# Optimization experiments

Measured on AMD Instinct MI355X. Metric: run time of the kernel, lower is better.

## Reference

```python
import jax, jax.numpy as jnp
import numpy as np

B, DM, E, P, K = 8192, 512, 4, 1024, 2
F = DM * E  # fused_input_dim = 2048


def setup_inputs() -> dict:
    key = jax.random.key(0)
    ks = jax.random.split(key, 8)
    return {
        "x_mod0": jax.random.normal(ks[0], (B, DM), jnp.float32),
        "x_mod1": jax.random.normal(ks[1], (B, DM), jnp.float32),
        "x_mod2": jax.random.normal(ks[2], (B, DM), jnp.float32),
        "x_mod3": jax.random.normal(ks[3], (B, DM), jnp.float32),
        "label": jax.random.normal(ks[4], (B, P), jnp.float32),
        "Wg": jax.random.normal(ks[5], (E, F), jnp.float32) * (1.0 / np.sqrt(F)),
        "We": jax.random.normal(ks[6], (E, F, P), jnp.float32) * (1.0 / np.sqrt(F)),
        "be": jax.random.normal(ks[7], (E, P), jnp.float32) * 0.01,
        "topk": K,
    }


def reference(x_mod0, x_mod1, x_mod2, x_mod3, label, Wg, We, be, topk):
    # fused = cat(modalities, dim=1)  -> [B, F]
    fused = jnp.concatenate([x_mod0, x_mod1, x_mod2, x_mod3], axis=1)
    # gate_scores = softmax(Linear(fused))  (Linear weight is [out,in], no bias)
    gate_scores = jax.nn.softmax(fused @ Wg.T, axis=-1)  # [B, E]
    top_k_values, top_k_indices = jax.lax.top_k(gate_scores, topk)  # [B, K]
    # Dense equivalent of per-sample expert dispatch: run every expert,
    # then gather the top-k expert outputs per token and weighted-sum them.
    all_out = jnp.einsum("bf,efp->bep", fused, We) + be  # [B, E, P]
    gathered = jnp.take_along_axis(all_out, top_k_indices[:, :, None], axis=1)  # [B, K, P]
    preds = jnp.sum(gathered * top_k_values[:, :, None], axis=1)  # [B, P]
    # loss_fn = MSE against x['label']
    loss = jnp.mean((preds - label) ** 2)
    return (loss, preds)
```

## Files before the change

kernel.cpp:

```cpp
#include <hip/hip_runtime.h>
#include <stdint.h>

#define Bsz  8192
#define DMOD 512
#define NE   4
#define NP   1024
#define NF   2048
#define BM   160
#define MAXTILES 57

typedef float  f32x4  __attribute__((ext_vector_type(4)));
typedef __bf16 bf16x8 __attribute__((ext_vector_type(8)));
typedef unsigned short u16x8 __attribute__((ext_vector_type(8)));

typedef __attribute__((address_space(3))) void       lds_void;
typedef const __attribute__((address_space(1))) void glb_void;
#define GLOAD16(gp, lp) \
  __builtin_amdgcn_global_load_lds((glb_void*)(gp), (lds_void*)(lp), 16, 0, 0)

__device__ __forceinline__ unsigned short f32_bf16(float f) {
  unsigned int u = __float_as_uint(f);
  u += 0x7FFFu + ((u >> 16) & 1u);
  return (unsigned short)(u >> 16);
}

__global__ __launch_bounds__(256) void gate_fuse(
    const float* __restrict__ x0, const float* __restrict__ x1,
    const float* __restrict__ x2, const float* __restrict__ x3,
    const float* __restrict__ Wg, const float* __restrict__ We,
    float* __restrict__ gw, int* __restrict__ pair,
    unsigned short* __restrict__ fusedB, unsigned short* __restrict__ WeT)
{
  __shared__ float sred[4][4];
  __shared__ float tsh[64][65];
  const int tid = threadIdx.x;

  if ((int)blockIdx.x < Bsz) {
    const int b = blockIdx.x;
    const int f = tid * 8;
    const float* xm  = (f < 1024) ? (f < 512 ? x0 : x1) : (f < 1536 ? x2 : x3);
    const float* src = xm + (size_t)b * DMOD + (f & 511);
    float4 v0 = *(const float4*)src;
    float4 v1 = *(const float4*)(src + 4);
    u16x8 o;
    o[0] = f32_bf16(v0.x); o[1] = f32_bf16(v0.y); o[2] = f32_bf16(v0.z); o[3] = f32_bf16(v0.w);
    o[4] = f32_bf16(v1.x); o[5] = f32_bf16(v1.y); o[6] = f32_bf16(v1.z); o[7] = f32_bf16(v1.w);
    *(u16x8*)(fusedB + (size_t)b * NF + f) = o;

    float d[4];
    #pragma unroll
    for (int e = 0; e < 4; ++e) {
      const float* w = Wg + e * NF + f;
      d[e] = v0.x * w[0] + v0.y * w[1] + v0.z * w[2] + v0.w * w[3]
           + v1.x * w[4] + v1.y * w[5] + v1.z * w[6] + v1.w * w[7];
    }
    #pragma unroll
    for (int off = 32; off; off >>= 1) {
      #pragma unroll
      for (int e = 0; e < 4; ++e) d[e] += __shfl_xor(d[e], off);
    }
    if ((tid & 63) == 0) {
      #pragma unroll
      for (int e = 0; e < 4; ++e) sred[tid >> 6][e] = d[e];
    }
    __syncthreads();
    if (tid == 0) {
      float a0 = sred[0][0] + sred[1][0] + sred[2][0] + sred[3][0];
      float a1 = sred[0][1] + sred[1][1] + sred[2][1] + sred[3][1];
      float a2 = sred[0][2] + sred[1][2] + sred[2][2] + sred[3][2];
      float a3 = sred[0][3] + sred[1][3] + sred[2][3] + sred[3][3];
      float m  = fmaxf(fmaxf(a0, a1), fmaxf(a2, a3));
      float e0 = expf(a0 - m), e1 = expf(a1 - m), e2 = expf(a2 - m), e3 = expf(a3 - m);
      float inv = 1.f / (e0 + e1 + e2 + e3);
      float p0 = e0 * inv, p1 = e1 * inv, p2 = e2 * inv, p3 = e3 * inv;
      int i1 = 0; float b1 = a0;
      if (a1 > b1) { b1 = a1; i1 = 1; }
      if (a2 > b1) { b1 = a2; i1 = 2; }
      if (a3 > b1) { b1 = a3; i1 = 3; }
      int i2 = -1; float b2 = -3.4e38f;
      if (i1 != 0 && a0 > b2) { b2 = a0; i2 = 0; }
      if (i1 != 1 && a1 > b2) { b2 = a1; i2 = 1; }
      if (i1 != 2 && a2 > b2) { b2 = a2; i2 = 2; }
      if (i1 != 3 && a3 > b2) { b2 = a3; i2 = 3; }
      gw[(size_t)b * 4 + 0] = (i1 == 0 || i2 == 0) ? p0 : 0.f;
      gw[(size_t)b * 4 + 1] = (i1 == 1 || i2 == 1) ? p1 : 0.f;
      gw[(size_t)b * 4 + 2] = (i1 == 2 || i2 == 2) ? p2 : 0.f;
      gw[(size_t)b * 4 + 3] = (i1 == 3 || i2 == 3) ? p3 : 0.f;
      int lo = min(i1, i2), hi = max(i1, i2);
      pair[b] = (lo == 0) ? (hi - 1) : (lo == 1) ? (hi + 1) : 5;
    }
  } else {
    const int tb = (int)blockIdx.x - Bsz;
    const int e  = tb >> 9;
    const int rem = tb & 511;
    const int tf = (rem & 31) * 64;
    const int tp = (rem >> 5) * 64;
    const int t4 = tid * 4;
    const float* src = We + ((size_t)e * NF + tf) * NP + tp;
    #pragma unroll
    for (int i = 0; i < 4; ++i) {
      int li = i * 1024 + t4;
      int r = li >> 6, c = li & 63;
      float4 v = *(const float4*)(src + (size_t)r * NP + c);
      tsh[c][r] = v.x; tsh[c+1][r] = v.y; tsh[c+2][r] = v.z; tsh[c+3][r] = v.w;
    }
    __syncthreads();
    unsigned short* dst = WeT + ((size_t)e * NP + tp) * NF + tf;
    #pragma unroll
    for (int i = 0; i < 4; ++i) {
      int li = i * 1024 + t4;
      int r = li >> 6, c = li & 63;
      ushort4 o;
      o.x = f32_bf16(tsh[r][c]);   o.y = f32_bf16(tsh[r][c+1]);
      o.z = f32_bf16(tsh[r][c+2]); o.w = f32_bf16(tsh[r][c+3]);
      *(ushort4*)(dst + (size_t)r * NF + c) = o;
    }
  }
}

__global__ __launch_bounds__(256) void bucket_scan(
    const int* __restrict__ pair, int* __restrict__ ridx,
    int4* __restrict__ tiletab, int* __restrict__ ntiles,
    double* __restrict__ lossAcc)
{
  __shared__ int cntS[256][6];
  __shared__ int baseS[6];
  const int tid = threadIdx.x;
  int c[6] = {0, 0, 0, 0, 0, 0};
  for (int i = 0; i < 32; ++i) {
    const int code = pair[tid * 32 + i];
    #pragma unroll
    for (int b = 0; b < 6; ++b) c[b] += (code == b) ? 1 : 0;
  }
  #pragma unroll
  for (int b = 0; b < 6; ++b) cntS[tid][b] = c[b];
  __syncthreads();
  if (tid < 6) {
    int run = 0;
    for (int i = 0; i < 256; ++i) { const int v = cntS[i][tid]; cntS[i][tid] = run; run += v; }
    baseS[tid] = run;
  }
  __syncthreads();
  if (tid == 0) {
    const int e1t[6] = {0, 0, 0, 1, 1, 2};
    const int e2t[6] = {1, 2, 3, 2, 3, 3};
    int base[6];
    int off = 0, nt = 0;
    for (int b = 0; b < 6; ++b) {
      base[b] = off;
      const int cb = baseS[b];
      for (int i = 0; i < cb; i += BM)
        tiletab[nt++] = make_int4(off + i, min(BM, cb - i), e1t[b], e2t[b]);
      off += cb;
    }
    *ntiles = nt;
    *lossAcc = 0.0;
    #pragma unroll
    for (int b = 0; b < 6; ++b) baseS[b] = base[b];
  }
  __syncthreads();
  int pos[6];
  #pragma unroll
  for (int b = 0; b < 6; ++b) pos[b] = baseS[b] + cntS[tid][b];
  for (int i = 0; i < 32; ++i) {
    const int r = tid * 32 + i;
    const int code = pair[r];
    #pragma unroll
    for (int b = 0; b < 6; ++b)
      if (code == b) { ridx[pos[b]] = r; ++pos[b]; }
  }
}

__global__ __launch_bounds__(512, 4) void moe_gemm_db(
    const unsigned short* __restrict__ fusedB,
    const unsigned short* __restrict__ WeT,
    const float* __restrict__ gw,
    const float* __restrict__ be,
    const float* __restrict__ label,
    const int* __restrict__ ntilesP,
    const int4* __restrict__ tiletab,
    const int* __restrict__ ridx,
    float* __restrict__ out,
    double* __restrict__ lossAcc)
{
  const int bid  = (int)blockIdx.x;
  const int swz  = (bid & 7) * 57 + (bid >> 3);
  const int tile = swz >> 3;
  if (tile >= *ntilesP) return;
  const int pcol = (swz & 7) * 128;

  __shared__ __align__(16) unsigned short As[2][BM * 32];
  __shared__ __align__(16) unsigned short B1s[2][128 * 32];
  __shared__ __align__(16) unsigned short B2s[2][128 * 32];
  __shared__ int   ridxS[BM];
  __shared__ float gwS[BM][2];
  __shared__ float red[8];

  const int4 te     = tiletab[tile];
  const int rowbase = te.x;
  const int vcount  = te.y;
  const int e1      = te.z;
  const int e2      = te.w;

  const int tid  = threadIdx.x;
  const int l    = tid & 63;
  const int wave = tid >> 6;
  const int wr   = wave >> 2;
  const int wc   = wave & 3;
  const int lrow = l & 15;
  const int g4   = l >> 4;
  const int schA = (l & 3) ^ ((l >> 3) & 3);

  if (tid < BM) {
    const int ri = ridx[rowbase + min(tid, vcount - 1)];
    ridxS[tid]  = ri;
    gwS[tid][0] = gw[(size_t)ri * 4 + e1];
    gwS[tid][1] = gw[(size_t)ri * 4 + e2];
  }
  __syncthreads();

  const int rowA0 = ridxS[wave * 16 + (l >> 2)];
  const int rowA1 = (wave < 2) ? ridxS[(8 + wave) * 16 + (l >> 2)] : 0;

  f32x4 acc1[5][2], acc2[5][2];
  #pragma unroll
  for (int m = 0; m < 5; ++m)
    #pragma unroll
    for (int n = 0; n < 2; ++n) {
      acc1[m][n] = f32x4{0.f, 0.f, 0.f, 0.f};
      acc2[m][n] = f32x4{0.f, 0.f, 0.f, 0.f};
    }

  auto STAGE = [&](int t, int buf) {
    const int k0 = t << 5;
    const unsigned short* B1g = WeT + ((size_t)e1 * NP + pcol) * NF + k0;
    const unsigned short* B2g = WeT + ((size_t)e2 * NP + pcol) * NF + k0;
    #pragma unroll
    for (int s = 0; s < 4; ++s) {
      const int idx = wave + s * 8;
      if (idx >= 26) continue;
      if (idx < 10) {
        const int r0  = idx * 16;
        const int row = (s == 0) ? rowA0 : rowA1;
        GLOAD16(fusedB + (size_t)row * NF + k0 + schA * 8, (char*)(&As[buf][r0 * 32]));
      } else if (idx < 18) {
        const int r0 = (idx - 10) * 16;
        GLOAD16(B1g + (size_t)(r0 + (l >> 2)) * NF + schA * 8, (char*)(&B1s[buf][r0 * 32]));
      } else {
        const int r0 = (idx - 18) * 16;
        GLOAD16(B2g + (size_t)(r0 + (l >> 2)) * NF + schA * 8, (char*)(&B2s[buf][r0 * 32]));
      }
    }
  };

  auto COMPUTE = [&](int buf) {
    bf16x8 af[5], b1f[2], b2f[2];
    #pragma unroll
    for (int m = 0; m < 5; ++m) {
      const int fr = wr * 80 + m * 16 + lrow;
      const int ch = (g4 ^ ((fr >> 1) & 3)) * 8;
      af[m] = __builtin_bit_cast(bf16x8, *(const u16x8*)(&As[buf][fr * 32 + ch]));
    }
    #pragma unroll
    for (int n = 0; n < 2; ++n) {
      const int fr = wc * 32 + n * 16 + lrow;
      const int ch = (g4 ^ ((fr >> 1) & 3)) * 8;
      b1f[n] = __builtin_bit_cast(bf16x8, *(const u16x8*)(&B1s[buf][fr * 32 + ch]));
      b2f[n] = __builtin_bit_cast(bf16x8, *(const u16x8*)(&B2s[buf][fr * 32 + ch]));
    }
    #pragma unroll
    for (int m = 0; m < 5; ++m)
      #pragma unroll
      for (int n = 0; n < 2; ++n) {
        acc1[m][n] = __builtin_amdgcn_mfma_f32_16x16x32_bf16(af[m], b1f[n], acc1[m][n], 0, 0, 0);
        acc2[m][n] = __builtin_amdgcn_mfma_f32_16x16x32_bf16(af[m], b2f[n], acc2[m][n], 0, 0, 0);
      }
  };

  STAGE(0, 0);
  STAGE(1, 1);

  #pragma unroll 1
  for (int t = 0; t < 64; ++t) {
    const int buf = t & 1;
    if (t == 63)       { asm volatile("s_waitcnt vmcnt(0)" ::: "memory"); }
    else if (wave < 2) { asm volatile("s_waitcnt vmcnt(4)" ::: "memory"); }
    else               { asm volatile("s_waitcnt vmcnt(3)" ::: "memory"); }
    __builtin_amdgcn_s_barrier();
    COMPUTE(buf);
    __builtin_amdgcn_sched_barrier(0);
    __builtin_amdgcn_s_barrier();
    if (t < 62) STAGE(t + 2, buf);
  }

  float lsum = 0.f;
  #pragma unroll
  for (int m = 0; m < 5; ++m) {
    #pragma unroll
    for (int r = 0; r < 4; ++r) {
      const int lrowi = wr * 80 + m * 16 + g4 * 4 + r;
      const bool valid = lrowi < vcount;
      const int grow = ridxS[lrowi];
      const float w1 = gwS[lrowi][0];
      const float w2 = gwS[lrowi][1];
      #pragma unroll
      for (int n = 0; n < 2; ++n) {
        const int gcol = pcol + wc * 32 + n * 16 + lrow;
        float pred = w1 * (acc1[m][n][r] + be[e1 * NP + gcol])
                   + w2 * (acc2[m][n][r] + be[e2 * NP + gcol]);
        if (valid) {
          out[1 + (size_t)grow * NP + gcol] = pred;
          float d = pred - label[(size_t)grow * NP + gcol];
          lsum += d * d;
        }
      }
    }
  }
  #pragma unroll
  for (int off = 32; off; off >>= 1) lsum += __shfl_xor(lsum, off);
  if (l == 0) red[wave] = lsum;
  __syncthreads();
  if (tid == 0) {
    double s = 0.0;
    #pragma unroll
    for (int w = 0; w < 8; ++w) s += (double)red[w];
    atomicAdd(lossAcc, s);
  }
}

__global__ void finalize_kernel(const double* __restrict__ lossAcc, float* __restrict__ out) {
  out[0] = (float)(*lossAcc * (1.0 / ((double)Bsz * (double)NP)));
}

extern "C" void kernel_launch(void* const* d_in, const int* in_sizes, int n_in,
                              void* d_out, int out_size, void* d_ws, size_t ws_size,
                              hipStream_t stream) {
  const float* x0    = (const float*)d_in[0];
  const float* x1    = (const float*)d_in[1];
  const float* x2    = (const float*)d_in[2];
  const float* x3    = (const float*)d_in[3];
  const float* label = (const float*)d_in[4];
  const float* Wg    = (const float*)d_in[5];
  const float* We    = (const float*)d_in[6];
  const float* be    = (const float*)d_in[7];
  float* out = (float*)d_out;

  char* ws = (char*)d_ws;
  unsigned short* WeT    = (unsigned short*)ws;
  unsigned short* fusedB = (unsigned short*)(ws + ((size_t)16 << 20));
  float*  gw      = (float*)(ws + ((size_t)48 << 20));
  char*   misc    = ws + ((size_t)49 << 20);
  double* lossAcc = (double*)(misc + 0);
  int*    ntiles  = (int*)(misc + 64);
  int4*   tiletab = (int4*)(misc + 256);
  int*    pair    = (int*)(misc + 4096);
  int*    ridx    = (int*)(misc + 4096 + 32768);

  gate_fuse<<<dim3(Bsz + 2048), 256, 0, stream>>>(x0, x1, x2, x3, Wg, We, gw, pair, fusedB, WeT);
  bucket_scan<<<dim3(1), 256, 0, stream>>>(pair, ridx, tiletab, ntiles, lossAcc);
  moe_gemm_db<<<dim3(MAXTILES * 8), 512, 0, stream>>>(
      fusedB, WeT, gw, be, label, ntiles, tiletab, ridx, out, lossAcc);
  finalize_kernel<<<1, 1, 0, stream>>>(lossAcc, out);
}
```

Measured before the change: 141.7 us.

## Triple-buffer GEMM LDS stages to drop per-iteration barrier; parallelize bucket scan

```diff
diff --git a/kernel.cpp b/kernel.cpp
--- a/kernel.cpp
+++ b/kernel.cpp
@@ -124,6 +124,7 @@
     double* __restrict__ lossAcc)
 {
   __shared__ int cntS[256][6];
+  __shared__ int segS[8][6];
   __shared__ int baseS[6];
   const int tid = threadIdx.x;
   int c[6] = {0, 0, 0, 0, 0, 0};
@@ -135,9 +136,19 @@
   #pragma unroll
   for (int b = 0; b < 6; ++b) cntS[tid][b] = c[b];
   __syncthreads();
+  if (tid < 48) {
+    const int b = tid >> 3, seg = tid & 7;
+    int run = 0;
+    for (int i = seg * 32; i < seg * 32 + 32; ++i) {
+      const int v = cntS[i][b]; cntS[i][b] = run; run += v;
+    }
+    segS[seg][b] = run;
+  }
+  __syncthreads();
   if (tid < 6) {
     int run = 0;
-    for (int i = 0; i < 256; ++i) { const int v = cntS[i][tid]; cntS[i][tid] = run; run += v; }
+    #pragma unroll
+    for (int s = 0; s < 8; ++s) { const int v = segS[s][tid]; segS[s][tid] = run; run += v; }
     baseS[tid] = run;
   }
   __syncthreads();
@@ -161,7 +172,7 @@
   __syncthreads();
   int pos[6];
   #pragma unroll
-  for (int b = 0; b < 6; ++b) pos[b] = baseS[b] + cntS[tid][b];
+  for (int b = 0; b < 6; ++b) pos[b] = baseS[b] + segS[tid >> 5][b] + cntS[tid][b];
   for (int i = 0; i < 32; ++i) {
     const int r = tid * 32 + i;
     const int code = pair[r];
@@ -189,9 +200,9 @@
   if (tile >= *ntilesP) return;
   const int pcol = (swz & 7) * 128;
 
-  __shared__ __align__(16) unsigned short As[2][BM * 32];
-  __shared__ __align__(16) unsigned short B1s[2][128 * 32];
-  __shared__ __align__(16) unsigned short B2s[2][128 * 32];
+  __shared__ __align__(16) unsigned short As[3][BM * 32];
+  __shared__ __align__(16) unsigned short B1s[3][128 * 32];
+  __shared__ __align__(16) unsigned short B2s[3][128 * 32];
   __shared__ int   ridxS[BM];
   __shared__ float gwS[BM][2];
   __shared__ float red[8];
@@ -231,7 +242,7 @@
       acc2[m][n] = f32x4{0.f, 0.f, 0.f, 0.f};
     }
 
-  auto STAGE = [&](int t, int buf) {
+  auto STAGE = [&](int t, unsigned short* Ad, unsigned short* B1d, unsigned short* B2d) {
     const int k0 = t << 5;
     const unsigned short* B1g = WeT + ((size_t)e1 * NP + pcol) * NF + k0;
     const unsigned short* B2g = WeT + ((size_t)e2 * NP + pcol) * NF + k0;
@@ -242,31 +253,32 @@
       if (idx < 10) {
         const int r0  = idx * 16;
         const int row = (s == 0) ? rowA0 : rowA1;
-        GLOAD16(fusedB + (size_t)row * NF + k0 + schA * 8, (char*)(&As[buf][r0 * 32]));
+        GLOAD16(fusedB + (size_t)row * NF + k0 + schA * 8, (char*)(Ad + r0 * 32));
       } else if (idx < 18) {
         const int r0 = (idx - 10) * 16;
-        GLOAD16(B1g + (size_t)(r0 + (l >> 2)) * NF + schA * 8, (char*)(&B1s[buf][r0 * 32]));
+        GLOAD16(B1g + (size_t)(r0 + (l >> 2)) * NF + schA * 8, (char*)(B1d + r0 * 32));
       } else {
         const int r0 = (idx - 18) * 16;
-        GLOAD16(B2g + (size_t)(r0 + (l >> 2)) * NF + schA * 8, (char*)(&B2s[buf][r0 * 32]));
+        GLOAD16(B2g + (size_t)(r0 + (l >> 2)) * NF + schA * 8, (char*)(B2d + r0 * 32));
       }
     }
   };
 
-  auto COMPUTE = [&](int buf) {
+  auto COMPUTE = [&](const unsigned short* Ar, const unsigned short* B1r,
+                     const unsigned short* B2r) {
     bf16x8 af[5], b1f[2], b2f[2];
     #pragma unroll
     for (int m = 0; m < 5; ++m) {
       const int fr = wr * 80 + m * 16 + lrow;
       const int ch = (g4 ^ ((fr >> 1) & 3)) * 8;
-      af[m] = __builtin_bit_cast(bf16x8, *(const u16x8*)(&As[buf][fr * 32 + ch]));
+      af[m] = __builtin_bit_cast(bf16x8, *(const u16x8*)(Ar + fr * 32 + ch));
     }
     #pragma unroll
     for (int n = 0; n < 2; ++n) {
       const int fr = wc * 32 + n * 16 + lrow;
       const int ch = (g4 ^ ((fr >> 1) & 3)) * 8;
-      b1f[n] = __builtin_bit_cast(bf16x8, *(const u16x8*)(&B1s[buf][fr * 32 + ch]));
-      b2f[n] = __builtin_bit_cast(bf16x8, *(const u16x8*)(&B2s[buf][fr * 32 + ch]));
+      b1f[n] = __builtin_bit_cast(bf16x8, *(const u16x8*)(B1r + fr * 32 + ch));
+      b2f[n] = __builtin_bit_cast(bf16x8, *(const u16x8*)(B2r + fr * 32 + ch));
     }
     #pragma unroll
     for (int m = 0; m < 5; ++m)
@@ -277,20 +289,25 @@
       }
   };
 
-  STAGE(0, 0);
-  STAGE(1, 1);
+  unsigned short *A0 = As[0],  *A1 = As[1],  *A2 = As[2];
+  unsigned short *B10 = B1s[0], *B11 = B1s[1], *B12 = B1s[2];
+  unsigned short *B20 = B2s[0], *B21 = B2s[1], *B22 = B2s[2];
+
+  STAGE(0, A0, B10, B20);
+  STAGE(1, A1, B11, B21);
 
   #pragma unroll 1
   for (int t = 0; t < 64; ++t) {
-    const int buf = t & 1;
     if (t == 63)       { asm volatile("s_waitcnt vmcnt(0)" ::: "memory"); }
     else if (wave < 2) { asm volatile("s_waitcnt vmcnt(4)" ::: "memory"); }
     else               { asm volatile("s_waitcnt vmcnt(3)" ::: "memory"); }
     __builtin_amdgcn_s_barrier();
-    COMPUTE(buf);
     __builtin_amdgcn_sched_barrier(0);
-    __builtin_amdgcn_s_barrier();
-    if (t < 62) STAGE(t + 2, buf);
+    if (t < 62) STAGE(t + 2, A2, B12, B22);
+    COMPUTE(A0, B10, B20);
+    unsigned short* ta = A0; A0 = A1; A1 = A2; A2 = ta;
+    unsigned short* t1 = B10; B10 = B11; B11 = B12; B12 = t1;
+    unsigned short* t2 = B20; B20 = B21; B21 = B22; B22 = t2;
   }
 
   float lsum = 0.f;
```

Result: slower. 150.0 us (+5.8%).
